# Optimization experiments

Measured on AMD Instinct MI355X. Metric: run time of the kernel, lower is better.

## Reference

```python
import jax, jax.numpy as jnp
import numpy as np

N, F, H, B = 8192, 128, 64, 8


def setup_inputs() -> dict:
    key = jax.random.key(0)
    ks = jax.random.split(key, 8)
    x = jax.random.normal(ks[0], (N, F), jnp.float32)
    pos = jax.random.normal(ks[1], (N, 3), jnp.float32)
    batch = jnp.sort(jax.random.randint(ks[2], (N,), 0, B)).astype(jnp.int64)
    cell = jax.random.normal(ks[3], (B, 3, 3), jnp.float32)
    # charge-head MLP params (Linear(F,H) -> SiLU -> Linear(H,1))
    W1 = jax.random.normal(ks[4], (F, H), jnp.float32) * (1.0 / np.sqrt(F))
    b1 = jnp.zeros((H,), jnp.float32)
    W2 = jax.random.normal(ks[5], (H, 1), jnp.float32) * (1.0 / np.sqrt(H))
    b2 = jnp.zeros((1,), jnp.float32)
    screening = jnp.float32(0.2)   # screening_init
    softening = jnp.float32(0.5)   # softening_init
    return {"x": x, "pos": pos, "cell": cell, "W1": W1, "b1": b1,
            "W2": W2, "b2": b2, "screening": screening,
            "softening": softening, "batch": batch}


def reference(x, pos, cell, W1, b1, W2, b2, screening, softening, batch):
    n_graphs = cell.shape[0]
    n = pos.shape[0]
    # latent scalar charge per atom
    h = jax.nn.silu(x @ W1 + b1)                       # [N,H]
    q = (h @ W2 + b2)[:, 0]                            # [N]
    # neutralize: subtract per-graph mean charge
    counts = jnp.clip(jax.ops.segment_sum(jnp.ones_like(q), batch,
                                          num_segments=n_graphs), 1.0)
    mean_q = jax.ops.segment_sum(q, batch, num_segments=n_graphs) / counts
    q = q - mean_q[batch]
    # dense all-pairs screened Coulomb (nonperiodic)
    delta = pos[None, :, :] - pos[:, None, :]          # [N,N,3]
    r = jnp.sqrt(jnp.sum(delta * delta, axis=-1) + softening * softening)
    kern = jnp.exp(-screening * r) / r                 # [N,N]
    same_graph = batch[None, :] == batch[:, None]
    idx = jnp.arange(n)
    mask = same_graph & (idx[None, :] != idx[:, None])
    kern = jnp.where(mask, kern, 0.0)
    pair_energy = 0.5 * (q[:, None] * q[None, :]) * kern
    atom_energy = jnp.sum(pair_energy, axis=1, keepdims=True)  # [N,1]
    return atom_energy
```

## Files before the change

### kernel.cpp

```cpp
#include <hip/hip_runtime.h>
#include <math.h>

#define NATOMS 8192
#define NF 128
#define NH 64
#define NB 8

#define TI 16
#define TJ 256
#define JS 16

#define OFF_BATCH32 0
#define OFF_Q       32768
#define OFF_GSTART  65536

__global__ __launch_bounds__(256) void fused1_kernel(
    const float* __restrict__ x, const float* __restrict__ W1,
    const float* __restrict__ b1, const float* __restrict__ W2,
    const float* __restrict__ b2, const void* __restrict__ batch_raw,
    int* __restrict__ batch32, int* __restrict__ gstart,
    float* __restrict__ q) {
    const int* v32 = (const int*)batch_raw;
    const long long* v64 = (const long long*)batch_raw;
    const int tid = threadIdx.x;

    if (blockIdx.x == 2048) {
        const bool is64 = (v32[NATOMS - 1] == 0);
        if (tid <= NB) {
            if (tid == NB) {
                gstart[NB] = NATOMS;
            } else {
                int lo = 0, hi = NATOMS;
                while (lo < hi) {
                    int mid = (lo + hi) >> 1;
                    int v = is64 ? (int)v64[mid] : v32[mid];
                    if (v < tid) lo = mid + 1; else hi = mid;
                }
                gstart[tid] = lo;
            }
        }
        return;
    }

    const int gt = blockIdx.x * 256 + tid;
    if (gt < NATOMS) {
        const bool is64 = (v32[NATOMS - 1] == 0);
        batch32[gt] = is64 ? (int)v64[gt] : v32[gt];
    }

    const int atom = gt >> 6;
    const int lane = tid & 63;

    const float* xr = x + atom * NF;
    float z0 = b1[lane], z1 = 0.0f;
#pragma unroll
    for (int f0 = 0; f0 < NF; f0 += 8) {
        const float4 xa = *(const float4*)(xr + f0);
        const float4 xb = *(const float4*)(xr + f0 + 4);
        z0 = fmaf(xa.x, W1[(f0 + 0) * NH + lane], z0);
        z1 = fmaf(xa.y, W1[(f0 + 1) * NH + lane], z1);
        z0 = fmaf(xa.z, W1[(f0 + 2) * NH + lane], z0);
        z1 = fmaf(xa.w, W1[(f0 + 3) * NH + lane], z1);
        z0 = fmaf(xb.x, W1[(f0 + 4) * NH + lane], z0);
        z1 = fmaf(xb.y, W1[(f0 + 5) * NH + lane], z1);
        z0 = fmaf(xb.z, W1[(f0 + 6) * NH + lane], z0);
        z1 = fmaf(xb.w, W1[(f0 + 7) * NH + lane], z1);
    }
    const float z = z0 + z1;
    const float h = z / (1.0f + __expf(-z));
    float t = h * W2[lane];
#pragma unroll
    for (int m = 32; m >= 1; m >>= 1) t += __shfl_xor(t, m, 64);
    if (lane == 0) q[atom] = t + b2[0];
}

__global__ __launch_bounds__(256) void pairfin_kernel(
    const float* __restrict__ pos, const float* __restrict__ q,
    const int* __restrict__ batch32, const int* __restrict__ gstart,
    float* __restrict__ out,
    const float* __restrict__ scr_p, const float* __restrict__ soft_p) {
    __shared__ float4 tile[TJ];
    __shared__ float smean[NB];
    __shared__ float red[4];
    __shared__ float psum[JS * TI];

    const int tid = threadIdx.x;
    const int ii = tid & (TI - 1);
    const int js = tid >> 4;

    const int i0 = blockIdx.x * TI;
    const int gfirst = batch32[i0];
    const int glast = batch32[i0 + TI - 1];

    for (int g = gfirst; g <= glast; ++g) {
        const int s = gstart[g], e = gstart[g + 1];
        float t = 0.0f;
        for (int idx = s + tid; idx < e; idx += 256) t += q[idx];
#pragma unroll
        for (int m = 32; m >= 1; m >>= 1) t += __shfl_xor(t, m, 64);
        if ((tid & 63) == 0) red[tid >> 6] = t;
        __syncthreads();
        if (tid == 0) {
            const int c = e - s;
            smean[g] = (red[0] + red[1] + red[2] + red[3]) /
                       (float)(c > 0 ? c : 1);
        }
        __syncthreads();
    }

    const float scr = *scr_p;
    const float soft = *soft_p;
    const float soft2 = soft * soft;

    const int i = i0 + ii;
    const int gi = batch32[i];
    const int si = gstart[gi];
    const unsigned span = (unsigned)(gstart[gi + 1] - si);
    const float pix = pos[3 * i + 0];
    const float piy = pos[3 * i + 1];
    const float piz = pos[3 * i + 2];

    const int jlo = gstart[gfirst];
    const int jhi = gstart[glast + 1];

    float acc = 0.0f;
    for (int jt = jlo; jt < jhi; jt += TJ) {
        __syncthreads();
        const int jj = jt + tid;
        float4 v;
        if (jj < jhi) {
            v.x = pos[3 * jj + 0];
            v.y = pos[3 * jj + 1];
            v.z = pos[3 * jj + 2];
            v.w = q[jj] - smean[batch32[jj]];
        } else {
            v.x = v.y = v.z = v.w = 0.0f;
        }
        tile[tid] = v;
        __syncthreads();

        const int cnt = min(TJ, jhi - jt);
        const int base = jt - si;
        const int ue = min(js * TI + TI, cnt);
        for (int u = js * TI; u < ue; ++u) {
            const float4 p = tile[u];
            const float dx = p.x - pix;
            const float dy = p.y - piy;
            const float dz = p.z - piz;
            float d2 = fmaf(dx, dx, soft2);
            d2 = fmaf(dy, dy, d2);
            d2 = fmaf(dz, dz, d2);
            const float rinv = rsqrtf(d2);
            const float r = d2 * rinv;
            const float e = __expf(-scr * r);
            const float w = ((unsigned)(base + u) < span) ? p.w : 0.0f;
            acc = fmaf(w * e, rinv, acc);
        }
    }
    psum[js * TI + ii] = acc;
    __syncthreads();

    if (tid < TI) {
        float tot = 0.0f;
#pragma unroll
        for (int k = 0; k < JS; ++k) tot += psum[k * TI + tid];
        const float qn = q[i] - smean[gi];
        const float sa = fabsf(soft);
        const float selfk = __expf(-scr * sa) / sa;
        out[i] = 0.5f * qn * (tot - qn * selfk);
    }
}

extern "C" void kernel_launch(void* const* d_in, const int* in_sizes, int n_in,
                              void* d_out, int out_size, void* d_ws, size_t ws_size,
                              hipStream_t stream) {
    const float* x    = (const float*)d_in[0];
    const float* pos  = (const float*)d_in[1];
    const float* W1   = (const float*)d_in[3];
    const float* b1   = (const float*)d_in[4];
    const float* W2   = (const float*)d_in[5];
    const float* b2   = (const float*)d_in[6];
    const float* scr  = (const float*)d_in[7];
    const float* soft = (const float*)d_in[8];
    const void*  braw = (const void*)d_in[9];

    char* ws = (char*)d_ws;
    int*   batch32 = (int*)(ws + OFF_BATCH32);
    float* q       = (float*)(ws + OFF_Q);
    int*   gstart  = (int*)(ws + OFF_GSTART);
    float* out     = (float*)d_out;

    fused1_kernel<<<2049, 256, 0, stream>>>(x, W1, b1, W2, b2, braw,
                                            batch32, gstart, q);
    pairfin_kernel<<<NATOMS / TI, 256, 0, stream>>>(pos, q, batch32, gstart,
                                                    out, scr, soft);
}
```

Before: 106.4 us.

## Fuse charge MLP and pair kernel into one cooperative kernel with grid sync

```diff
diff --git a/kernel.cpp b/kernel.cpp
--- a/kernel.cpp
+++ b/kernel.cpp
@@ -1,5 +1,8 @@
 #include <hip/hip_runtime.h>
+#include <hip/hip_cooperative_groups.h>
 #include <math.h>
+
+namespace cg = cooperative_groups;
 
 #define NATOMS 8192
 #define NF 128
@@ -14,70 +17,13 @@
 #define OFF_Q       32768
 #define OFF_GSTART  65536
 
-__global__ __launch_bounds__(256) void fused1_kernel(
+__global__ __launch_bounds__(256, 2) void fused_all_kernel(
     const float* __restrict__ x, const float* __restrict__ W1,
     const float* __restrict__ b1, const float* __restrict__ W2,
     const float* __restrict__ b2, const void* __restrict__ batch_raw,
+    const float* __restrict__ pos,
     int* __restrict__ batch32, int* __restrict__ gstart,
-    float* __restrict__ q) {
-    const int* v32 = (const int*)batch_raw;
-    const long long* v64 = (const long long*)batch_raw;
-    const int tid = threadIdx.x;
-
-    if (blockIdx.x == 2048) {
-        const bool is64 = (v32[NATOMS - 1] == 0);
-        if (tid <= NB) {
-            if (tid == NB) {
-                gstart[NB] = NATOMS;
-            } else {
-                int lo = 0, hi = NATOMS;
-                while (lo < hi) {
-                    int mid = (lo + hi) >> 1;
-                    int v = is64 ? (int)v64[mid] : v32[mid];
-                    if (v < tid) lo = mid + 1; else hi = mid;
-                }
-                gstart[tid] = lo;
-            }
-        }
-        return;
-    }
-
-    const int gt = blockIdx.x * 256 + tid;
-    if (gt < NATOMS) {
-        const bool is64 = (v32[NATOMS - 1] == 0);
-        batch32[gt] = is64 ? (int)v64[gt] : v32[gt];
-    }
-
-    const int atom = gt >> 6;
-    const int lane = tid & 63;
-
-    const float* xr = x + atom * NF;
-    float z0 = b1[lane], z1 = 0.0f;
-#pragma unroll
-    for (int f0 = 0; f0 < NF; f0 += 8) {
-        const float4 xa = *(const float4*)(xr + f0);
-        const float4 xb = *(const float4*)(xr + f0 + 4);
-        z0 = fmaf(xa.x, W1[(f0 + 0) * NH + lane], z0);
-        z1 = fmaf(xa.y, W1[(f0 + 1) * NH + lane], z1);
-        z0 = fmaf(xa.z, W1[(f0 + 2) * NH + lane], z0);
-        z1 = fmaf(xa.w, W1[(f0 + 3) * NH + lane], z1);
-        z0 = fmaf(xb.x, W1[(f0 + 4) * NH + lane], z0);
-        z1 = fmaf(xb.y, W1[(f0 + 5) * NH + lane], z1);
-        z0 = fmaf(xb.z, W1[(f0 + 6) * NH + lane], z0);
-        z1 = fmaf(xb.w, W1[(f0 + 7) * NH + lane], z1);
-    }
-    const float z = z0 + z1;
-    const float h = z / (1.0f + __expf(-z));
-    float t = h * W2[lane];
-#pragma unroll
-    for (int m = 32; m >= 1; m >>= 1) t += __shfl_xor(t, m, 64);
-    if (lane == 0) q[atom] = t + b2[0];
-}
-
-__global__ __launch_bounds__(256) void pairfin_kernel(
-    const float* __restrict__ pos, const float* __restrict__ q,
-    const int* __restrict__ batch32, const int* __restrict__ gstart,
-    float* __restrict__ out,
+    float* __restrict__ q, float* __restrict__ out,
     const float* __restrict__ scr_p, const float* __restrict__ soft_p) {
     __shared__ float4 tile[TJ];
     __shared__ float smean[NB];
@@ -85,13 +31,86 @@
     __shared__ float psum[JS * TI];
 
     const int tid = threadIdx.x;
-    const int ii = tid & (TI - 1);
-    const int js = tid >> 4;
-
-    const int i0 = blockIdx.x * TI;
+    const int bid = blockIdx.x;
+    const int i0 = bid * TI;
+
+    const int* v32 = (const int*)batch_raw;
+    const long long* v64 = (const long long*)batch_raw;
+    const bool is64 = (v32[NATOMS - 1] == 0);
+
+    if (tid < TI) {
+        const int a = i0 + tid;
+        batch32[a] = is64 ? (int)v64[a] : v32[a];
+    }
+    if (bid == 0 && tid <= NB) {
+        if (tid == NB) {
+            gstart[NB] = NATOMS;
+        } else {
+            int lo = 0, hi = NATOMS;
+            while (lo < hi) {
+                int mid = (lo + hi) >> 1;
+                int v = is64 ? (int)v64[mid] : v32[mid];
+                if (v < tid) lo = mid + 1; else hi = mid;
+            }
+            gstart[tid] = lo;
+        }
+    }
+
+    {
+        const int wave = tid >> 6;
+        const int lane = tid & 63;
+        const int a0 = i0 + wave * 4;
+        const float* xr0 = x + (a0 + 0) * NF;
+        const float* xr1 = x + (a0 + 1) * NF;
+        const float* xr2 = x + (a0 + 2) * NF;
+        const float* xr3 = x + (a0 + 3) * NF;
+        const float bb = b1[lane];
+        float z0 = bb, z1 = bb, z2 = bb, z3 = bb;
+#pragma unroll
+        for (int f = 0; f < NF; f += 4) {
+            const float4 xa = *(const float4*)(xr0 + f);
+            const float4 xb = *(const float4*)(xr1 + f);
+            const float4 xc = *(const float4*)(xr2 + f);
+            const float4 xd = *(const float4*)(xr3 + f);
+            const float w0 = W1[(f + 0) * NH + lane];
+            const float w1 = W1[(f + 1) * NH + lane];
+            const float w2 = W1[(f + 2) * NH + lane];
+            const float w3 = W1[(f + 3) * NH + lane];
+            z0 = fmaf(xa.x, w0, z0); z1 = fmaf(xb.x, w0, z1);
+            z2 = fmaf(xc.x, w0, z2); z3 = fmaf(xd.x, w0, z3);
+            z0 = fmaf(xa.y, w1, z0); z1 = fmaf(xb.y, w1, z1);
+            z2 = fmaf(xc.y, w1, z2); z3 = fmaf(xd.y, w1, z3);
+            z0 = fmaf(xa.z, w2, z0); z1 = fmaf(xb.z, w2, z1);
+            z2 = fmaf(xc.z, w2, z2); z3 = fmaf(xd.z, w2, z3);
+            z0 = fmaf(xa.w, w3, z0); z1 = fmaf(xb.w, w3, z1);
+            z2 = fmaf(xc.w, w3, z2); z3 = fmaf(xd.w, w3, z3);
+        }
+        const float wl = W2[lane];
+        float t0 = wl * (z0 / (1.0f + __expf(-z0)));
+        float t1 = wl * (z1 / (1.0f + __expf(-z1)));
+        float t2 = wl * (z2 / (1.0f + __expf(-z2)));
+        float t3 = wl * (z3 / (1.0f + __expf(-z3)));
+#pragma unroll
+        for (int m = 32; m >= 1; m >>= 1) {
+            t0 += __shfl_xor(t0, m, 64);
+            t1 += __shfl_xor(t1, m, 64);
+            t2 += __shfl_xor(t2, m, 64);
+            t3 += __shfl_xor(t3, m, 64);
+        }
+        if (lane == 0) {
+            const float bo = b2[0];
+            q[a0 + 0] = t0 + bo;
+            q[a0 + 1] = t1 + bo;
+            q[a0 + 2] = t2 + bo;
+            q[a0 + 3] = t3 + bo;
+        }
+    }
+
+    __threadfence();
+    cg::this_grid().sync();
+
     const int gfirst = batch32[i0];
     const int glast = batch32[i0 + TI - 1];
-
     for (int g = gfirst; g <= glast; ++g) {
         const int s = gstart[g], e = gstart[g + 1];
         float t = 0.0f;
@@ -112,6 +131,8 @@
     const float soft = *soft_p;
     const float soft2 = soft * soft;
 
+    const int ii = tid & (TI - 1);
+    const int js = tid >> 4;
     const int i = i0 + ii;
     const int gi = batch32[i];
     const int si = gstart[gi];
@@ -190,8 +211,10 @@
     int*   gstart  = (int*)(ws + OFF_GSTART);
     float* out     = (float*)d_out;
 
-    fused1_kernel<<<2049, 256, 0, stream>>>(x, W1, b1, W2, b2, braw,
-                                            batch32, gstart, q);
-    pairfin_kernel<<<NATOMS / TI, 256, 0, stream>>>(pos, q, batch32, gstart,
-                                                    out, scr, soft);
+    void* args[] = {(void*)&x, (void*)&W1, (void*)&b1, (void*)&W2,
+                    (void*)&b2, (void*)&braw, (void*)&pos,
+                    (void*)&batch32, (void*)&gstart, (void*)&q,
+                    (void*)&out, (void*)&scr, (void*)&soft};
+    hipLaunchCooperativeKernel((void*)fused_all_kernel, dim3(NATOMS / TI),
+                               dim3(256), args, 0, stream);
 }
```

After: 184.4 us. 1.73x slower.
